# Optimization experiments

Hardware: AMD Instinct MI355X
Metric: run time of the kernel (lower is better)

The kernel has to match this reference:

```python
import jax, jax.numpy as jnp
import numpy as np

N_NODES = 10000
N_EDGES = 160000
IN_F = 512
H_F = 512
OUT_F = 512


def _graph_conv(x, W, b, src, dst, norm_out, norm_in):
    # DGL GraphConv, norm='both': out = D_in^{-1/2} A D_out^{-1/2} X W + b
    xs = x * norm_out[:, None]            # scale src features by out-deg^-1/2
    msgs = xs[src]                        # gather: [E, F]
    agg = jax.ops.segment_sum(msgs, dst, num_segments=N_NODES)  # scatter-sum
    agg = agg * norm_in[:, None]          # scale by in-deg^-1/2
    return agg @ W + b


def setup_inputs() -> dict:
    key = jax.random.key(0)
    ks = jax.random.split(key, 10)
    inputs = jax.random.normal(ks[0], (N_NODES, IN_F), dtype=jnp.float32)
    src = jax.random.randint(ks[1], (N_EDGES,), 0, N_NODES, dtype=jnp.int32)
    dst = jax.random.randint(ks[2], (N_EDGES,), 0, N_NODES, dtype=jnp.int32)
    # Glorot-ish init for GraphConv weights, zero bias (DGL default)
    def glorot(k, fan_in, fan_out):
        s = jnp.sqrt(6.0 / (fan_in + fan_out)).astype(jnp.float32)
        return jax.random.uniform(k, (fan_in, fan_out), jnp.float32, -s, s)
    W1 = glorot(ks[3], IN_F, H_F)
    b1 = jnp.zeros((H_F,), jnp.float32)
    W2 = glorot(ks[4], H_F, H_F)
    b2 = jnp.zeros((H_F,), jnp.float32)
    W3 = glorot(ks[5], H_F, OUT_F)
    b3 = jnp.zeros((OUT_F,), jnp.float32)
    return {"inputs": inputs, "W1": W1, "b1": b1, "W2": W2, "b2": b2,
            "W3": W3, "b3": b3, "src": src, "dst": dst}


def reference(inputs, W1, b1, W2, b2, W3, b3, src, dst):
    ones = jnp.ones((N_EDGES,), jnp.float32)
    deg_out = jax.ops.segment_sum(ones, src, num_segments=N_NODES)
    deg_in = jax.ops.segment_sum(ones, dst, num_segments=N_NODES)
    norm_out = jnp.where(deg_out > 0, deg_out ** -0.5, 0.0)
    norm_in = jnp.where(deg_in > 0, deg_in ** -0.5, 0.0)

    h1 = jax.nn.relu(_graph_conv(inputs, W1, b1, src, dst, norm_out, norm_in))
    h2 = jax.nn.relu(_graph_conv(h1, W2, b2, src, dst, norm_out, norm_in))
    # NOTE: original module applies gcn_layer_2 a second time here (not layer 3)
    h3 = jax.nn.relu(_graph_conv(h2, W2, b2, src, dst, norm_out, norm_in))
    h4 = _graph_conv(h2, W3, b3, src, dst, norm_out, norm_in)
    return (h4, h3, h2)
```

## Files before the change

kernel.cpp:

```cpp
#include <hip/hip_runtime.h>

#define N_NODES 10000
#define N_EDGES 160000
#define FEAT 512
#define M_PAD 10048
#define QSTRIDE 1286144

typedef unsigned int uint32;

typedef __attribute__((ext_vector_type(8))) _Float16 half8;
typedef __attribute__((ext_vector_type(4))) float f32x4;


__device__ __forceinline__ void load_lds16(const void* g, void* l) {
    __builtin_amdgcn_global_load_lds(
        (const __attribute__((address_space(1))) void*)g,
        (__attribute__((address_space(3))) void*)l, 16, 0, 0);
}

__global__ void deg_kernel(const int* __restrict__ src, const int* __restrict__ dst,
                           int* __restrict__ deg_out, int* __restrict__ deg_in) {
    int e = blockIdx.x * blockDim.x + threadIdx.x;
    if (e < N_EDGES) {
        atomicAdd(&deg_out[src[e]], 1);
        atomicAdd(&deg_in[dst[e]], 1);
    }
}

__global__ __launch_bounds__(256) void scan1_kernel(const int* __restrict__ deg_in,
        const int* __restrict__ deg_out, int* __restrict__ row_ptr,
        int* __restrict__ bsum, float* __restrict__ norm_out, float* __restrict__ norm_in) {
    __shared__ int s[256];
    int t = threadIdx.x, b = blockIdx.x;
    int i = b * 256 + t;
    int v = (i < N_NODES) ? deg_in[i] : 0;
    s[t] = v;
    __syncthreads();
    for (int off = 1; off < 256; off <<= 1) {
        int x = (t >= off) ? s[t - off] : 0;
        __syncthreads();
        s[t] += x;
        __syncthreads();
    }
    if (i < N_NODES) {
        row_ptr[i] = s[t] - v;
        int dob = deg_out[i];
        norm_in[i]  = v   > 0 ? rsqrtf((float)v)   : 0.f;
        norm_out[i] = dob > 0 ? rsqrtf((float)dob) : 0.f;
    }
    if (t == 255) bsum[b] = s[255];
}

__global__ __launch_bounds__(256) void scan2_kernel(const int* __restrict__ bsum,
        int* __restrict__ row_ptr, int* __restrict__ cursor) {
    int t = threadIdx.x, b = blockIdx.x;
    int i = b * 256 + t;
    int off = 0;
    for (int j = 0; j < b; j++) off += bsum[j];
    if (i < N_NODES) {
        int r = row_ptr[i] + off;
        row_ptr[i] = r;
        cursor[i] = r;
    }
    if (b == 0 && t == 0) row_ptr[N_NODES] = N_EDGES;
}

__global__ void fill_kernel(const int* __restrict__ src, const int* __restrict__ dst,
                            int* __restrict__ cursor, int* __restrict__ edge_src) {
    int e = blockIdx.x * blockDim.x + threadIdx.x;
    if (e < N_EDGES) {
        int d = dst[e];
        int pos = atomicAdd(&cursor[d], 1);
        edge_src[pos] = src[e];
    }
}

__global__ __launch_bounds__(256) void prescale_kernel(const float* __restrict__ x,
        const float* __restrict__ norm_out, _Float16* __restrict__ xs) {
    int idx = blockIdx.x * 256 + threadIdx.x;
    if (idx >= N_NODES * 64) return;
    int node = idx >> 6, f8 = idx & 63;
    float w = norm_out[node];
    const float4* p = (const float4*)&x[(size_t)node * 512 + f8 * 8];
    float4 a = p[0], b = p[1];
    half8 h;
    h[0] = (_Float16)(a.x * w); h[1] = (_Float16)(a.y * w);
    h[2] = (_Float16)(a.z * w); h[3] = (_Float16)(a.w * w);
    h[4] = (_Float16)(b.x * w); h[5] = (_Float16)(b.y * w);
    h[6] = (_Float16)(b.z * w); h[7] = (_Float16)(b.w * w);
    int q = f8 >> 4, fl8 = f8 & 15;
    *(half8*)&xs[(size_t)q * QSTRIDE + (size_t)node * 128 + fl8 * 8] = h;
}

__global__ __launch_bounds__(64) void agg_kernel(const _Float16* __restrict__ xs,
        const int* __restrict__ edge_src, const int* __restrict__ row_ptr,
        const float* __restrict__ norm_in, _Float16* __restrict__ a_t) {
    int bid = blockIdx.x;
    int xcd = bid & 7;
    int q = xcd >> 1;
    int d = ((bid >> 3) << 1) | (xcd & 1);
    int lane = threadIdx.x;
    int fl = lane & 15, g = lane >> 4;
    float acc[8] = {};
    if (d < N_NODES) {
        int beg = row_ptr[d], end = row_ptr[d + 1];
        const _Float16* xq = xs + (size_t)q * QSTRIDE + fl * 8;
        int e = beg + g;
        for (; e + 12 < end; e += 16) {
            int s0 = edge_src[e],     s1 = edge_src[e + 4];
            int s2 = edge_src[e + 8], s3 = edge_src[e + 12];
            half8 v0 = *(const half8*)&xq[(size_t)s0 * 128];
            half8 v1 = *(const half8*)&xq[(size_t)s1 * 128];
            half8 v2 = *(const half8*)&xq[(size_t)s2 * 128];
            half8 v3 = *(const half8*)&xq[(size_t)s3 * 128];
#pragma unroll
            for (int i = 0; i < 8; i++)
                acc[i] += ((float)v0[i] + (float)v1[i]) + ((float)v2[i] + (float)v3[i]);
        }
        for (; e + 4 < end; e += 8) {
            int s0 = edge_src[e], s1 = edge_src[e + 4];
            half8 v0 = *(const half8*)&xq[(size_t)s0 * 128];
            half8 v1 = *(const half8*)&xq[(size_t)s1 * 128];
#pragma unroll
            for (int i = 0; i < 8; i++) acc[i] += (float)v0[i] + (float)v1[i];
        }
        for (; e < end; e += 4) {
            int s = edge_src[e];
            half8 v = *(const half8*)&xq[(size_t)s * 128];
#pragma unroll
            for (int i = 0; i < 8; i++) acc[i] += (float)v[i];
        }
#pragma unroll
        for (int i = 0; i < 8; i++) {
            acc[i] += __shfl_xor(acc[i], 16);
            acc[i] += __shfl_xor(acc[i], 32);
        }
        float ni = norm_in[d];
#pragma unroll
        for (int i = 0; i < 8; i++) acc[i] *= ni;
    }
    if (g == 0) {
        half8 h8;
#pragma unroll
        for (int i = 0; i < 8; i++) h8[i] = (_Float16)acc[i];
        size_t o = (size_t)(d >> 4) * 8192 + (size_t)(q * 4 + (fl >> 2)) * 512
                 + (size_t)((fl & 3) * 16 + (d & 15)) * 8;
        *(half8*)&a_t[o] = h8;
    }
}

__global__ __launch_bounds__(256) void wsplit_kernel(const float* __restrict__ W1,
        const float* __restrict__ W2, const float* __restrict__ W3,
        _Float16* __restrict__ wt) {
    const float* W = blockIdx.y == 0 ? W1 : (blockIdx.y == 1 ? W2 : W3);
    size_t mbase = (size_t)blockIdx.y * 262144;
    int chunk = blockIdx.x * 256 + threadIdx.x;
    int i = chunk & 63;
    int kb = (chunk >> 6) & 15;
    int s = chunk >> 10;
    int n = s * 16 + (i & 15);
    int k0 = kb * 32 + (i >> 4) * 8;
    half8 h8;
#pragma unroll
    for (int j = 0; j < 8; j++)
        h8[j] = (_Float16)W[(size_t)(k0 + j) * 512 + n];
    *(half8*)&wt[mbase + (size_t)chunk * 8] = h8;
}

template <bool RELU_A, bool RELU_B, bool WRITE_C, bool WRITE_XS>
__global__ __launch_bounds__(256) void mfma_gemm(
        const _Float16* __restrict__ A_t, const _Float16* __restrict__ Bt,
        const float* __restrict__ bias_a, const float* __restrict__ bias_b,
        const float* __restrict__ norm_out,
        float* __restrict__ Ca, float* __restrict__ Cb,
        _Float16* __restrict__ xs) {
    __shared__ __align__(16) _Float16 lsA[64 * 32];
    __shared__ __align__(16) _Float16 lsB[128 * 32];
    int tid = threadIdx.x;
    int w = tid >> 6, lane = tid & 63;
    int col0 = blockIdx.x * 128;
    int row0 = blockIdx.y * 64;
    int wm = w & 1, wn = w >> 1;
    int lr = lane & 15, lq = lane >> 4;

    size_t aoff = (size_t)((row0 >> 4) + w) * 8192 + lane * 8;
    size_t boff = (size_t)((col0 >> 4) + 2 * w) * 8192 + lane * 8;
    _Float16* dA  = &lsA[(w * 64 + lane) * 8];
    _Float16* dB0 = &lsB[((2 * w) * 64 + lane) * 8];
    _Float16* dB1 = &lsB[((2 * w + 1) * 64 + lane) * 8];

    f32x4 acc[2][4] = {};

    for (int kb = 0; kb < 16; kb++) {
        size_t ko = (size_t)kb * 512;
        load_lds16(A_t + aoff + ko, dA);
        load_lds16(Bt + boff + ko, dB0);
        load_lds16(Bt + boff + 8192 + ko, dB1);
        __syncthreads();

        half8 a[2], b[4];
#pragma unroll
        for (int i = 0; i < 2; i++)
            a[i] = *(const half8*)&lsA[((wm * 2 + i) * 64 + lane) * 8];
#pragma unroll
        for (int j = 0; j < 4; j++)
            b[j] = *(const half8*)&lsB[((wn * 4 + j) * 64 + lane) * 8];
#pragma unroll
        for (int i = 0; i < 2; i++)
#pragma unroll
            for (int j = 0; j < 4; j++)
                acc[i][j] = __builtin_amdgcn_mfma_f32_16x16x32_f16(a[i], b[j], acc[i][j], 0, 0, 0);
        __syncthreads();
    }

    bool sec = (col0 >= 512);
    const float* bias = sec ? bias_b : bias_a;
    float* C = sec ? Cb : Ca;
    int cb0 = sec ? col0 - 512 : col0;
    const bool relu = sec ? RELU_B : RELU_A;

#pragma unroll
    for (int i = 0; i < 2; i++)
#pragma unroll
        for (int j = 0; j < 4; j++) {
            int col = cb0 + wn * 64 + j * 16 + lr;
            float bv = bias[col];
#pragma unroll
            for (int r = 0; r < 4; r++) {
                int row = row0 + wm * 32 + i * 16 + lq * 4 + r;
                if (row < N_NODES) {
                    float v = acc[i][j][r] + bv;
                    if (relu) v = fmaxf(v, 0.f);
                    if (WRITE_C) C[(size_t)row * 512 + col] = v;
                    if (WRITE_XS) {
                        int q = col >> 7, f = col & 127;
                        xs[(size_t)q * QSTRIDE + (size_t)row * 128 + f] =
                            (_Float16)(v * norm_out[row]);
                    }
                }
            }
        }
}

extern "C" void kernel_launch(void* const* d_in, const int* in_sizes, int n_in,
                              void* d_out, int out_size, void* d_ws, size_t ws_size,
                              hipStream_t stream) {
    const float* x  = (const float*)d_in[0];
    const float* W1 = (const float*)d_in[1];
    const float* b1 = (const float*)d_in[2];
    const float* W2 = (const float*)d_in[3];
    const float* b2 = (const float*)d_in[4];
    const float* W3 = (const float*)d_in[5];
    const float* b3 = (const float*)d_in[6];
    const int* src  = (const int*)d_in[7];
    const int* dst  = (const int*)d_in[8];
    float* out = (float*)d_out;

    int* wsi = (int*)d_ws;
    int* deg_out  = wsi;
    int* deg_in   = wsi + 10000;
    float* norm_out = (float*)(wsi + 20000);
    float* norm_in  = (float*)(wsi + 30000);
    int* row_ptr  = wsi + 40000;
    int* cursor   = wsi + 50016;
    int* bsum     = wsi + 60016;
    int* edge_src = wsi + 60064;
    _Float16* wt  = (_Float16*)(wsi + 220064);
    _Float16* a_t = wt + 786432;
    _Float16* xs  = a_t + (size_t)M_PAD * 512;

    float* h4 = out;
    float* h3 = out + 5120000;
    float* h2 = out + 10240000;

    hipMemsetAsync(d_ws, 0, 20000 * sizeof(int), stream);

    deg_kernel<<<(N_EDGES + 255) / 256, 256, 0, stream>>>(src, dst, deg_out, deg_in);
    scan1_kernel<<<40, 256, 0, stream>>>(deg_in, deg_out, row_ptr, bsum, norm_out, norm_in);
    scan2_kernel<<<40, 256, 0, stream>>>(bsum, row_ptr, cursor);
    fill_kernel<<<(N_EDGES + 255) / 256, 256, 0, stream>>>(src, dst, cursor, edge_src);
    wsplit_kernel<<<dim3(128, 3), 256, 0, stream>>>(W1, W2, W3, wt);
    prescale_kernel<<<(N_NODES * 64 + 255) / 256, 256, 0, stream>>>(x, norm_out, xs);

    _Float16* wt1 = wt;
    _Float16* wt2 = wt + 262144;

    dim3 ga(M_PAD * 4);
    dim3 g1(4, M_PAD / 64);
    dim3 g2(8, M_PAD / 64);

    agg_kernel<<<ga, 64, 0, stream>>>(xs, edge_src, row_ptr, norm_in, a_t);
    mfma_gemm<true, true, false, true><<<g1, 256, 0, stream>>>(
        a_t, wt1, b1, b1, norm_out, h2, h2, xs);
    agg_kernel<<<ga, 64, 0, stream>>>(xs, edge_src, row_ptr, norm_in, a_t);
    mfma_gemm<true, true, true, true><<<g1, 256, 0, stream>>>(
        a_t, wt2, b2, b2, norm_out, h2, h2, xs);
    agg_kernel<<<ga, 64, 0, stream>>>(xs, edge_src, row_ptr, norm_in, a_t);
    mfma_gemm<true, false, true, false><<<g2, 256, 0, stream>>>(
        a_t, wt2, b2, b3, norm_out, h3, h4, xs);
}
```

Before: 243.9 us.

## Pack four destination nodes per agg block and add 128-row GEMM for final layer

The aggregation kernel now runs 256-thread blocks, with each wavefront handling one destination node, so there are four times fewer blocks to schedule. The final dual-output GEMM uses a new 128x128 tile kernel that doubles A reuse per block and halves the number of row blocks. M_PAD grows to 10112 to fit the 128-row tiling. The changes trade scheduling overhead and reuse against lower occupancy and coarser load balancing, and they also shift the XCD-to-node mapping.

```diff
diff --git a/kernel.cpp b/kernel.cpp
--- a/kernel.cpp
+++ b/kernel.cpp
@@ -3,7 +3,7 @@
 #define N_NODES 10000
 #define N_EDGES 160000
 #define FEAT 512
-#define M_PAD 10048
+#define M_PAD 10112
 #define QSTRIDE 1286144
 
 typedef unsigned int uint32;
@@ -92,14 +92,16 @@
     *(half8*)&xs[(size_t)q * QSTRIDE + (size_t)node * 128 + fl8 * 8] = h;
 }
 
-__global__ __launch_bounds__(64) void agg_kernel(const _Float16* __restrict__ xs,
+__global__ __launch_bounds__(256) void agg_kernel(const _Float16* __restrict__ xs,
         const int* __restrict__ edge_src, const int* __restrict__ row_ptr,
         const float* __restrict__ norm_in, _Float16* __restrict__ a_t) {
     int bid = blockIdx.x;
     int xcd = bid & 7;
     int q = xcd >> 1;
-    int d = ((bid >> 3) << 1) | (xcd & 1);
-    int lane = threadIdx.x;
+    int grp = ((bid >> 3) << 1) | (xcd & 1);
+    int w = threadIdx.x >> 6;
+    int d = grp * 4 + w;
+    int lane = threadIdx.x & 63;
     int fl = lane & 15, g = lane >> 4;
     float acc[8] = {};
     if (d < N_NODES) {
@@ -167,13 +169,11 @@
     *(half8*)&wt[mbase + (size_t)chunk * 8] = h8;
 }
 
-template <bool RELU_A, bool RELU_B, bool WRITE_C, bool WRITE_XS>
-__global__ __launch_bounds__(256) void mfma_gemm(
+template <bool RELU_A, bool WRITE_C, bool WRITE_XS>
+__global__ __launch_bounds__(256) void mfma_gemm64(
         const _Float16* __restrict__ A_t, const _Float16* __restrict__ Bt,
-        const float* __restrict__ bias_a, const float* __restrict__ bias_b,
-        const float* __restrict__ norm_out,
-        float* __restrict__ Ca, float* __restrict__ Cb,
-        _Float16* __restrict__ xs) {
+        const float* __restrict__ bias_a, const float* __restrict__ norm_out,
+        float* __restrict__ Ca, _Float16* __restrict__ xs) {
     __shared__ __align__(16) _Float16 lsA[64 * 32];
     __shared__ __align__(16) _Float16 lsB[128 * 32];
     int tid = threadIdx.x;
@@ -213,30 +213,93 @@
         __syncthreads();
     }
 
-    bool sec = (col0 >= 512);
-    const float* bias = sec ? bias_b : bias_a;
-    float* C = sec ? Cb : Ca;
-    int cb0 = sec ? col0 - 512 : col0;
-    const bool relu = sec ? RELU_B : RELU_A;
-
 #pragma unroll
     for (int i = 0; i < 2; i++)
 #pragma unroll
         for (int j = 0; j < 4; j++) {
-            int col = cb0 + wn * 64 + j * 16 + lr;
-            float bv = bias[col];
+            int col = col0 + wn * 64 + j * 16 + lr;
+            float bv = bias_a[col];
 #pragma unroll
             for (int r = 0; r < 4; r++) {
                 int row = row0 + wm * 32 + i * 16 + lq * 4 + r;
                 if (row < N_NODES) {
                     float v = acc[i][j][r] + bv;
-                    if (relu) v = fmaxf(v, 0.f);
-                    if (WRITE_C) C[(size_t)row * 512 + col] = v;
+                    if (RELU_A) v = fmaxf(v, 0.f);
+                    if (WRITE_C) Ca[(size_t)row * 512 + col] = v;
                     if (WRITE_XS) {
                         int q = col >> 7, f = col & 127;
                         xs[(size_t)q * QSTRIDE + (size_t)row * 128 + f] =
                             (_Float16)(v * norm_out[row]);
                     }
+                }
+            }
+        }
+}
+
+__global__ __launch_bounds__(256) void mfma_gemm128(
+        const _Float16* __restrict__ A_t, const _Float16* __restrict__ Bt,
+        const float* __restrict__ bias_a, const float* __restrict__ bias_b,
+        float* __restrict__ Ca, float* __restrict__ Cb) {
+    __shared__ __align__(16) _Float16 lsA[128 * 32];
+    __shared__ __align__(16) _Float16 lsB[128 * 32];
+    int tid = threadIdx.x;
+    int w = tid >> 6, lane = tid & 63;
+    int col0 = blockIdx.x * 128;
+    int row0 = blockIdx.y * 128;
+    int wm = w & 1, wn = w >> 1;
+    int lr = lane & 15, lq = lane >> 4;
+
+    size_t aoff = (size_t)((row0 >> 4) + 2 * w) * 8192 + lane * 8;
+    size_t boff = (size_t)((col0 >> 4) + 2 * w) * 8192 + lane * 8;
+    _Float16* dA0 = &lsA[((2 * w) * 64 + lane) * 8];
+    _Float16* dA1 = dA0 + 512;
+    _Float16* dB0 = &lsB[((2 * w) * 64 + lane) * 8];
+    _Float16* dB1 = dB0 + 512;
+
+    f32x4 acc[4][4] = {};
+
+    for (int kb = 0; kb < 16; kb++) {
+        size_t ko = (size_t)kb * 512;
+        load_lds16(A_t + aoff + ko, dA0);
+        load_lds16(A_t + aoff + 8192 + ko, dA1);
+        load_lds16(Bt + boff + ko, dB0);
+        load_lds16(Bt + boff + 8192 + ko, dB1);
+        __syncthreads();
+
+        half8 a[4], b[4];
+#pragma unroll
+        for (int i = 0; i < 4; i++)
+            a[i] = *(const half8*)&lsA[((wm * 4 + i) * 64 + lane) * 8];
+#pragma unroll
+        for (int j = 0; j < 4; j++)
+            b[j] = *(const half8*)&lsB[((wn * 4 + j) * 64 + lane) * 8];
+#pragma unroll
+        for (int i = 0; i < 4; i++)
+#pragma unroll
+            for (int j = 0; j < 4; j++)
+                acc[i][j] = __builtin_amdgcn_mfma_f32_16x16x32_f16(a[i], b[j], acc[i][j], 0, 0, 0);
+        __syncthreads();
+    }
+
+    bool sec = (col0 >= 512);
+    const float* bias = sec ? bias_b : bias_a;
+    float* C = sec ? Cb : Ca;
+    int cb0 = sec ? col0 - 512 : col0;
+    const bool relu = !sec;
+
+#pragma unroll
+    for (int i = 0; i < 4; i++)
+#pragma unroll
+        for (int j = 0; j < 4; j++) {
+            int col = cb0 + wn * 64 + j * 16 + lr;
+            float bv = bias[col];
+#pragma unroll
+            for (int r = 0; r < 4; r++) {
+                int row = row0 + wm * 64 + i * 16 + lq * 4 + r;
+                if (row < N_NODES) {
+                    float v = acc[i][j][r] + bv;
+                    if (relu) v = fmaxf(v, 0.f);
+                    C[(size_t)row * 512 + col] = v;
                 }
             }
         }
@@ -285,17 +348,17 @@
     _Float16* wt1 = wt;
     _Float16* wt2 = wt + 262144;
 
-    dim3 ga(M_PAD * 4);
+    dim3 ga(M_PAD);
     dim3 g1(4, M_PAD / 64);
-    dim3 g2(8, M_PAD / 64);
-
-    agg_kernel<<<ga, 64, 0, stream>>>(xs, edge_src, row_ptr, norm_in, a_t);
-    mfma_gemm<true, true, false, true><<<g1, 256, 0, stream>>>(
-        a_t, wt1, b1, b1, norm_out, h2, h2, xs);
-    agg_kernel<<<ga, 64, 0, stream>>>(xs, edge_src, row_ptr, norm_in, a_t);
-    mfma_gemm<true, true, true, true><<<g1, 256, 0, stream>>>(
-        a_t, wt2, b2, b2, norm_out, h2, h2, xs);
-    agg_kernel<<<ga, 64, 0, stream>>>(xs, edge_src, row_ptr, norm_in, a_t);
-    mfma_gemm<true, false, true, false><<<g2, 256, 0, stream>>>(
-        a_t, wt2, b2, b3, norm_out, h3, h4, xs);
-}
+    dim3 g2(8, M_PAD / 128);
+
+    agg_kernel<<<ga, 256, 0, stream>>>(xs, edge_src, row_ptr, norm_in, a_t);
+    mfma_gemm64<true, false, true><<<g1, 256, 0, stream>>>(
+        a_t, wt1, b1, norm_out, h2, xs);
+    agg_kernel<<<ga, 256, 0, stream>>>(xs, edge_src, row_ptr, norm_in, a_t);
+    mfma_gemm64<true, true, true><<<g1, 256, 0, stream>>>(
+        a_t, wt2, b2, norm_out, h2, xs);
+    agg_kernel<<<ga, 256, 0, stream>>>(xs, edge_src, row_ptr, norm_in, a_t);
+    mfma_gemm128<<<g2, 256, 0, stream>>>(
+        a_t, wt2, b2, b3, h3, h4);
+}
```

New measurement: 251.2 us. 1.03x slower.
